# Performance work log

Hardware: AMD Instinct MI355X
Metric: run time of the kernel (lower is better)

The kernel has to match this reference:

```python
import jax, jax.numpy as jnp
import numpy as np

B, T, NM, DM, DI, DS, DR, DC, NC = 8, 512, 128, 512, 1024, 32, 32, 4, 100


def setup_inputs() -> dict:
    ks = jax.random.split(jax.random.key(0), 10)
    r = lambda i, shape, s: (jax.random.normal(ks[i], shape) * s).astype(jnp.float32)
    return {
        "x": jax.random.normal(ks[0], (B, T, NM), dtype=jnp.float32),
        "w_proj": r(1, (NM, DM), 0.05),
        "b_proj": jnp.zeros((DM,), jnp.float32),
        "rms_w": jnp.ones((DM,), jnp.float32),
        "w_in": r(2, (DM, 2 * DI), 0.02),
        "conv_w": r(3, (DI, 1, DC), 0.2),
        "conv_b": jnp.zeros((DI,), jnp.float32),
        "w_xproj": r(4, (DI, DR + 2 * DS), 0.02),
        "w_dt": r(5, (DR, DI), 0.1),
        "b_dt": jnp.full((DI,), -4.6, jnp.float32),  # softplus -> ~0.01 init dt
        "A_log": jnp.log(jnp.broadcast_to(jnp.arange(1, DS + 1, dtype=jnp.float32), (DI, DS))),
        "D": jnp.ones((DI,), jnp.float32),
        "w_out": r(6, (DI, DM), 0.02),
        "w_cls": r(7, (DM, NC), 0.05),
        "b_cls": jnp.zeros((NC,), jnp.float32),
    }


def _forward(x, w_proj, b_proj, rms_w, w_in, conv_w, conv_b, w_xproj, w_dt, b_dt,
             A_log, D, w_out, w_cls, b_cls):
    # LinearNorm input projection: (B,T,NM) -> (B,T,DM)
    h0 = x @ w_proj + b_proj
    # RMSNorm (pre-norm of the ResidualBlock)
    xn = h0 * jax.lax.rsqrt(jnp.mean(h0 * h0, axis=-1, keepdims=True) + 1e-5) * rms_w
    # MambaBlock: in_proj (no bias) -> split into ssm path and gate residual
    xr = xn @ w_in                       # (B,T,2*DI)
    xp, res = jnp.split(xr, 2, axis=-1)  # each (B,T,DI)
    # causal depthwise conv1d (torch pads d_conv-1 both sides then slices [:T])
    xc = jnp.transpose(xp, (0, 2, 1))    # (B,DI,T)
    xc = jax.lax.conv_general_dilated(
        xc, conv_w, window_strides=(1,), padding=((DC - 1, 0),),
        dimension_numbers=("NCH", "OIH", "NCH"), feature_group_count=DI)
    xc = xc + conv_b[None, :, None]
    xp = jax.nn.silu(jnp.transpose(xc, (0, 2, 1)))  # (B,T,DI)
    # input-dependent SSM parameters
    xdbl = xp @ w_xproj                              # (B,T,DR+2*DS)
    dt, Bm, Cm = jnp.split(xdbl, [DR, DR + DS], axis=-1)
    delta = jax.nn.softplus(dt @ w_dt + b_dt)        # (B,T,DI)
    A = -jnp.exp(A_log)                              # (DI,DS)

    # selective scan: h_t = exp(delta_t*A) h_{t-1} + (delta_t*u_t) B_t ; y_t = <h_t, C_t>
    def step(hprev, inp):
        d_t, B_t, C_t, u_t = inp                     # (B,DI),(B,DS),(B,DS),(B,DI)
        dA = jnp.exp(d_t[..., None] * A)             # (B,DI,DS)
        h = dA * hprev + (d_t * u_t)[..., None] * B_t[:, None, :]
        y = jnp.einsum("bds,bs->bd", h, C_t)
        return h, y

    xs = (jnp.swapaxes(delta, 0, 1), jnp.swapaxes(Bm, 0, 1),
          jnp.swapaxes(Cm, 0, 1), jnp.swapaxes(xp, 0, 1))
    h_init = jnp.zeros((B, DI, DS), dtype=x.dtype)
    _, ys = jax.lax.scan(step, h_init, xs)           # ys: (T,B,DI)
    y = jnp.swapaxes(ys, 0, 1) + xp * D              # skip term D*u
    y = y * jax.nn.silu(res)                         # gate
    enc = h0 + y @ w_out                             # residual add
    # NB: faithful to source: mean over dim=2 (feature dim) -> (B,T), T==DM
    pooled = jnp.mean(enc, axis=2)
    return pooled @ w_cls + b_cls                    # (B,NC)


def reference(x, w_proj, b_proj, rms_w, w_in, conv_w, conv_b, w_xproj, w_dt, b_dt,
              A_log, D, w_out, w_cls, b_cls):
    return _forward(x, w_proj, b_proj, rms_w, w_in, conv_w, conv_b, w_xproj,
                    w_dt, b_dt, A_log, D, w_out, w_cls, b_cls)
```

## Files before the change

kernel.cpp:

```cpp
#include <hip/hip_runtime.h>
#include <hip/hip_bf16.h>
#include <cstddef>

#define Bb 8
#define Tt 512
#define NM 128
#define DM 512
#define DI 1024
#define DS 32
#define DR 32
#define DC 4
#define NC 100
#define BT (Bb*Tt)
#define NCH 8
#define CL  64

typedef unsigned short ushort_t;
typedef unsigned int uint_t;
typedef __attribute__((ext_vector_type(8))) short bf8;
typedef __attribute__((ext_vector_type(4))) float f4;

__device__ __forceinline__ float softplus_f(float x) {
    return fmaxf(x, 0.f) + log1pf(expf(-fabsf(x)));
}
__device__ __forceinline__ float silu_fast(float x) {
    return __fdividef(x, 1.f + __expf(-x));
}
__device__ __forceinline__ ushort_t bf16_rne(float x) {
    uint_t u = __float_as_uint(x);
    uint_t r = u + 0x7FFFu + ((u >> 16) & 1u);
    return (ushort_t)(r >> 16);
}
__device__ __forceinline__ float bf16_tof(ushort_t h) {
    return __uint_as_float(((uint_t)h) << 16);
}
__device__ __forceinline__ uint_t packf(float v) {
    ushort_t h = bf16_rne(v);
    ushort_t l = bf16_rne(v - bf16_tof(h));
    return ((uint_t)h << 16) | (uint_t)l;
}
template<int CTRL>
__device__ __forceinline__ float qperm(float x) {
    return __int_as_float(__builtin_amdgcn_mov_dpp(__float_as_int(x), CTRL, 0xF, 0xF, true));
}
template<int PAT>
__device__ __forceinline__ float swz(float x) {
    return __int_as_float(__builtin_amdgcn_ds_swizzle(__float_as_int(x), PAT));
}

__global__ __launch_bounds__(256) void prep_kernel(
    const float* __restrict__ x, const float* __restrict__ w_in,
    const float* __restrict__ w_out, const float* __restrict__ w_xp,
    const float* __restrict__ w_pj, const float* __restrict__ w_dt,
    uint_t* __restrict__ x_pk,
    ushort_t* __restrict__ w_in_hi, ushort_t* __restrict__ w_in_lo,
    ushort_t* __restrict__ w_out_hi, ushort_t* __restrict__ w_out_lo,
    ushort_t* __restrict__ w_xp_hi, ushort_t* __restrict__ w_xp_lo,
    ushort_t* __restrict__ w_pj_hi, ushort_t* __restrict__ w_pj_lo,
    ushort_t* __restrict__ w_dt_hi, ushort_t* __restrict__ w_dt_lo,
    float4* __restrict__ zbase, int zcount)
{
    __shared__ ushort_t th[32][34], tl[32][34];
    const int bid = blockIdx.x;
    const float* src;
    ushort_t *hi, *lo;
    int K, N, bx, by;
    if (bid < 1024)      { src = w_in;  hi = w_in_hi;  lo = w_in_lo;  K = DM; N = 2 * DI; bx = bid & 63; by = bid >> 6; }
    else if (bid < 1536) { const int i = bid - 1024; src = w_out; hi = w_out_hi; lo = w_out_lo; K = DI; N = DM; bx = i & 15; by = i >> 4; }
    else if (bid < 1632) { const int i = bid - 1536; src = w_xp;  hi = w_xp_hi;  lo = w_xp_lo;  K = DI; N = 96; bx = i % 3; by = i / 3; }
    else if (bid < 1696) { const int i = bid - 1632; src = w_pj;  hi = w_pj_hi;  lo = w_pj_lo;  K = NM; N = DM; bx = i & 15; by = i >> 4; }
    else if (bid < 1728) { const int i = bid - 1696; src = w_dt;  hi = w_dt_hi;  lo = w_dt_lo;  K = DR; N = DI; bx = i; by = 0; }
    else {
        const int e = (bid - 1728) * 256 + threadIdx.x;
        x_pk[e] = packf(x[e]);
        if (e < zcount) zbase[e] = make_float4(0.f, 0.f, 0.f, 0.f);
        return;
    }
    const int k0 = by * 32, n0 = bx * 32;
    #pragma unroll
    for (int it = 0; it < 4; ++it) {
        const int idx = it * 256 + threadIdx.x;
        const int r = idx >> 5, c = idx & 31;
        const float v = src[(size_t)(k0 + r) * N + n0 + c];
        const ushort_t h = bf16_rne(v);
        th[c][r] = h;
        tl[c][r] = bf16_rne(v - bf16_tof(h));
    }
    __syncthreads();
    #pragma unroll
    for (int it = 0; it < 4; ++it) {
        const int idx = it * 256 + threadIdx.x;
        const int r = idx >> 5, c = idx & 31;
        hi[(size_t)(n0 + r) * K + k0 + c] = th[r][c];
        lo[(size_t)(n0 + r) * K + k0 + c] = tl[r][c];
    }
}

__global__ __launch_bounds__(512) void gemm_mfma_h0(
    const uint_t* __restrict__ Apk,
    const ushort_t* __restrict__ Bhi, const ushort_t* __restrict__ Blo,
    const float* __restrict__ bias, float* __restrict__ C)
{
    constexpr int BM = 128, BN = 128, FM = 2, FN = 4, K = NM, N = DM;
    __shared__ ushort_t sA[2][BM][40];
    __shared__ ushort_t sB[2][BN][40];
    const int tid = threadIdx.x;
    const int wid = tid >> 6, l = tid & 63, l15 = l & 15, g = l >> 4;
    const int wm = (wid >> 1) * 32, wn = (wid & 1) * 64;
    const int bm0 = blockIdx.y * BM, bn0 = blockIdx.x * BN;

    f4 acc[FM][FN] = {};
    uint4 aR[2], bRh, bRl;

    auto loadG = [&](int k0) {
        #pragma unroll
        for (int r = 0; r < 2; ++r) {
            const int idx = r * 2048 + tid * 4;
            const int m = idx >> 5, k = idx & 31;
            aR[r] = *(const uint4*)(Apk + (size_t)(bm0 + m) * K + k0 + k);
        }
        {
            const int idx = tid * 8;
            const int n = idx >> 5, k = idx & 31;
            const size_t o = (size_t)(bn0 + n) * K + k0 + k;
            bRh = *(const uint4*)(Bhi + o);
            bRl = *(const uint4*)(Blo + o);
        }
    };
    auto stoL = [&]() {
        #pragma unroll
        for (int r = 0; r < 2; ++r) {
            const int idx = r * 2048 + tid * 4;
            const int m = idx >> 5, k = idx & 31;
            uint2 hh, ll;
            hh.x = (aR[r].x >> 16) | (aR[r].y & 0xFFFF0000u);
            hh.y = (aR[r].z >> 16) | (aR[r].w & 0xFFFF0000u);
            ll.x = (aR[r].x & 0xFFFFu) | (aR[r].y << 16);
            ll.y = (aR[r].z & 0xFFFFu) | (aR[r].w << 16);
            *(uint2*)&sA[0][m][k] = hh;
            *(uint2*)&sA[1][m][k] = ll;
        }
        {
            const int idx = tid * 8;
            const int n = idx >> 5, k = idx & 31;
            *(uint4*)&sB[0][n][k] = bRh;
            *(uint4*)&sB[1][n][k] = bRl;
        }
    };

    loadG(0);
    for (int k0 = 0; k0 < K; k0 += 32) {
        stoL();
        __syncthreads();
        if (k0 + 32 < K) loadG(k0 + 32);
        bf8 ah[FM], al_[FM], bh[FN], bl_[FN];
        #pragma unroll
        for (int i = 0; i < FM; ++i) {
            ah[i]  = *(bf8*)&sA[0][wm + i * 16 + l15][g * 8];
            al_[i] = *(bf8*)&sA[1][wm + i * 16 + l15][g * 8];
        }
        #pragma unroll
        for (int j = 0; j < FN; ++j) {
            bh[j]  = *(bf8*)&sB[0][wn + j * 16 + l15][g * 8];
            bl_[j] = *(bf8*)&sB[1][wn + j * 16 + l15][g * 8];
        }
        #pragma unroll
        for (int i = 0; i < FM; ++i)
            #pragma unroll
            for (int j = 0; j < FN; ++j)
                acc[i][j] = __builtin_amdgcn_mfma_f32_16x16x32_bf16(ah[i], bh[j], acc[i][j], 0, 0, 0);
        #pragma unroll
        for (int i = 0; i < FM; ++i)
            #pragma unroll
            for (int j = 0; j < FN; ++j)
                acc[i][j] = __builtin_amdgcn_mfma_f32_16x16x32_bf16(al_[i], bh[j], acc[i][j], 0, 0, 0);
        #pragma unroll
        for (int i = 0; i < FM; ++i)
            #pragma unroll
            for (int j = 0; j < FN; ++j)
                acc[i][j] = __builtin_amdgcn_mfma_f32_16x16x32_bf16(ah[i], bl_[j], acc[i][j], 0, 0, 0);
        __syncthreads();
    }
    #pragma unroll
    for (int i = 0; i < FM; ++i)
        #pragma unroll
        for (int j = 0; j < FN; ++j)
            #pragma unroll
            for (int r = 0; r < 4; ++r) {
                const int m = bm0 + wm + i * 16 + g * 4 + r;
                const int n = bn0 + wn + j * 16 + l15;
                C[(size_t)m * N + n] = acc[i][j][r] + bias[n];
            }
}

__global__ __launch_bounds__(256) void gemm_mfma_dt(
    const float* __restrict__ xdbl,
    const ushort_t* __restrict__ Bhi, const ushort_t* __restrict__ Blo,
    const float* __restrict__ bias, float* __restrict__ dT)
{
    constexpr int FM = 2, FN = 2;
    __shared__ ushort_t sA[2][64][40];
    __shared__ ushort_t sB[2][64][40];
    const int tid = threadIdx.x;
    const int wid = tid >> 6, l = tid & 63, l15 = l & 15, g = l >> 4;
    const int wm = (wid >> 1) * 32, wn = (wid & 1) * 32;
    const int bm0 = blockIdx.y * 64, bn0 = blockIdx.x * 64;

    #pragma unroll
    for (int r = 0; r < 2; ++r) {
        const int idx = r * 1024 + tid * 4;
        const int m = idx >> 5, k = idx & 31;
        const float4 v = *(const float4*)(xdbl + (size_t)(bm0 + m) * 96 + k);
        const float vv[4] = {v.x, v.y, v.z, v.w};
        #pragma unroll
        for (int q = 0; q < 4; ++q) {
            const ushort_t h = bf16_rne(vv[q]);
            sA[0][m][k + q] = h;
            sA[1][m][k + q] = bf16_rne(vv[q] - bf16_tof(h));
        }
    }
    {
        const int idx = tid * 8;
        const int n = idx >> 5, k = idx & 31;
        *(uint4*)&sB[0][n][k] = *(const uint4*)(Bhi + (size_t)(bn0 + n) * 32 + k);
        *(uint4*)&sB[1][n][k] = *(const uint4*)(Blo + (size_t)(bn0 + n) * 32 + k);
    }
    __syncthreads();
    f4 acc[FM][FN] = {};
    bf8 ah[FM], al_[FM], bh[FN], bl_[FN];
    #pragma unroll
    for (int i = 0; i < FM; ++i) {
        ah[i]  = *(bf8*)&sA[0][wm + i * 16 + l15][g * 8];
        al_[i] = *(bf8*)&sA[1][wm + i * 16 + l15][g * 8];
    }
    #pragma unroll
    for (int j = 0; j < FN; ++j) {
        bh[j]  = *(bf8*)&sB[0][wn + j * 16 + l15][g * 8];
        bl_[j] = *(bf8*)&sB[1][wn + j * 16 + l15][g * 8];
    }
    #pragma unroll
    for (int i = 0; i < FM; ++i)
        #pragma unroll
        for (int j = 0; j < FN; ++j) {
            acc[i][j] = __builtin_amdgcn_mfma_f32_16x16x32_bf16(ah[i], bh[j], acc[i][j], 0, 0, 0);
            acc[i][j] = __builtin_amdgcn_mfma_f32_16x16x32_bf16(al_[i], bh[j], acc[i][j], 0, 0, 0);
            acc[i][j] = __builtin_amdgcn_mfma_f32_16x16x32_bf16(ah[i], bl_[j], acc[i][j], 0, 0, 0);
        }
    #pragma unroll
    for (int i = 0; i < FM; ++i)
        #pragma unroll
        for (int j = 0; j < FN; ++j) {
            const int n = bn0 + wn + j * 16 + l15;
            const int m0 = bm0 + wm + i * 16 + g * 4;
            const float bn = bias[n];
            float4 o;
            o.x = softplus_f(acc[i][j][0] + bn);
            o.y = softplus_f(acc[i][j][1] + bn);
            o.z = softplus_f(acc[i][j][2] + bn);
            o.w = softplus_f(acc[i][j][3] + bn);
            *(float4*)(dT + ((size_t)(m0 >> 9) * DI + n) * Tt + (m0 & 511)) = o;
        }
}

__global__ __launch_bounds__(512) void gemm_mfma_big(
    const uint_t* __restrict__ Apk, int lda,
    const ushort_t* __restrict__ Bhi,
    ushort_t* __restrict__ C, int N, int K)
{
    constexpr int FM = 2, FN = 4;
    __shared__ ushort_t sA[128][40];
    __shared__ ushort_t sB[128][40];
    const int tid = threadIdx.x;
    const int wid = tid >> 6, l = tid & 63, l15 = l & 15, g = l >> 4;
    const int wm = (wid >> 1) * 32, wn = (wid & 1) * 64;
    const int bm0 = blockIdx.y * 128, bn0 = blockIdx.x * 128;

    f4 acc[FM][FN] = {};
    uint4 aR[2], bRh;

    auto loadG = [&](int k0) {
        #pragma unroll
        for (int r = 0; r < 2; ++r) {
            const int idx = r * 2048 + tid * 4;
            const int m = idx >> 5, k = idx & 31;
            aR[r] = *(const uint4*)(Apk + (size_t)(bm0 + m) * lda + k0 + k);
        }
        {
            const int idx = tid * 8;
            const int n = idx >> 5, k = idx & 31;
            bRh = *(const uint4*)(Bhi + (size_t)(bn0 + n) * K + k0 + k);
        }
    };
    auto stoL = [&]() {
        #pragma unroll
        for (int r = 0; r < 2; ++r) {
            const int idx = r * 2048 + tid * 4;
            const int m = idx >> 5, k = idx & 31;
            uint2 hh;
            hh.x = (aR[r].x >> 16) | (aR[r].y & 0xFFFF0000u);
            hh.y = (aR[r].z >> 16) | (aR[r].w & 0xFFFF0000u);
            *(uint2*)&sA[m][k] = hh;
        }
        {
            const int idx = tid * 8;
            const int n = idx >> 5, k = idx & 31;
            *(uint4*)&sB[n][k] = bRh;
        }
    };

    loadG(0);
    for (int k0 = 0; k0 < K; k0 += 32) {
        stoL();
        __syncthreads();
        if (k0 + 32 < K) loadG(k0 + 32);
        bf8 ah[FM], bh[FN];
        #pragma unroll
        for (int i = 0; i < FM; ++i)
            ah[i] = *(bf8*)&sA[wm + i * 16 + l15][g * 8];
        #pragma unroll
        for (int j = 0; j < FN; ++j)
            bh[j] = *(bf8*)&sB[wn + j * 16 + l15][g * 8];
        #pragma unroll
        for (int i = 0; i < FM; ++i)
            #pragma unroll
            for (int j = 0; j < FN; ++j)
                acc[i][j] = __builtin_amdgcn_mfma_f32_16x16x32_bf16(ah[i], bh[j], acc[i][j], 0, 0, 0);
        __syncthreads();
    }
    #pragma unroll
    for (int i = 0; i < FM; ++i)
        #pragma unroll
        for (int j = 0; j < FN; ++j)
            #pragma unroll
            for (int r = 0; r < 4; ++r) {
                const int m = bm0 + wm + i * 16 + g * 4 + r;
                const int n = bn0 + wn + j * 16 + l15;
                C[(size_t)m * N + n] = bf16_rne(acc[i][j][r]);
            }
}

__global__ __launch_bounds__(256) void gemm_mfma_x(
    const ushort_t* __restrict__ Abf,
    const ushort_t* __restrict__ Bhi,
    float* __restrict__ C, int K, int kseg)
{
    constexpr int FM = 2, FN = 3;
    __shared__ ushort_t sAx[64][40];
    __shared__ ushort_t sBx[96][40];
    const int tid = threadIdx.x;
    const int wid = tid >> 6, l = tid & 63, l15 = l & 15, g = l >> 4;
    const int wm = (wid >> 1) * 32, wn = (wid & 1) * 48;
    const int bm0 = blockIdx.y * 64;
    const int kbeg = blockIdx.z * kseg;

    f4 acc[FM][FN] = {};
    uint4 aR;
    uint2 bRh[3];

    auto loadG = [&](int k0) {
        {
            const int idx = tid * 8;
            const int m = idx >> 5, k = idx & 31;
            aR = *(const uint4*)(Abf + (size_t)(bm0 + m) * K + k0 + k);
        }
        #pragma unroll
        for (int r = 0; r < 3; ++r) {
            const int idx = r * 1024 + tid * 4;
            const int n = idx >> 5, k = idx & 31;
            bRh[r] = *(const uint2*)(Bhi + (size_t)n * K + k0 + k);
        }
    };
    auto stoL = [&]() {
        {
            const int idx = tid * 8;
            const int m = idx >> 5, k = idx & 31;
            *(uint4*)&sAx[m][k] = aR;
        }
        #pragma unroll
        for (int r = 0; r < 3; ++r) {
            const int idx = r * 1024 + tid * 4;
            const int n = idx >> 5, k = idx & 31;
            *(uint2*)&sBx[n][k] = bRh[r];
        }
    };

    loadG(kbeg);
    for (int k0 = kbeg; k0 < kbeg + kseg; k0 += 32) {
        stoL();
        __syncthreads();
        if (k0 + 32 < kbeg + kseg) loadG(k0 + 32);
        bf8 ah[FM], bh[FN];
        #pragma unroll
        for (int i = 0; i < FM; ++i)
            ah[i] = *(bf8*)&sAx[wm + i * 16 + l15][g * 8];
        #pragma unroll
        for (int j = 0; j < FN; ++j)
            bh[j] = *(bf8*)&sBx[wn + j * 16 + l15][g * 8];
        #pragma unroll
        for (int i = 0; i < FM; ++i)
            #pragma unroll
            for (int j = 0; j < FN; ++j)
                acc[i][j] = __builtin_amdgcn_mfma_f32_16x16x32_bf16(ah[i], bh[j], acc[i][j], 0, 0, 0);
        __syncthreads();
    }
    #pragma unroll
    for (int i = 0; i < FM; ++i)
        #pragma unroll
        for (int j = 0; j < FN; ++j)
            #pragma unroll
            for (int r = 0; r < 4; ++r) {
                const int m = bm0 + wm + i * 16 + g * 4 + r;
                const int n = wn + j * 16 + l15;
                unsafeAtomicAdd(&C[(size_t)m * 96 + n], acc[i][j][r]);
            }
}

__global__ __launch_bounds__(256) void gemm_mfma_pool(
    const uint_t* __restrict__ Apk, int lda,
    const ushort_t* __restrict__ Bhi,
    float* __restrict__ pooled, float pscale,
    int N, int K, int kseg)
{
    constexpr int FM = 2, FN = 2;
    __shared__ ushort_t sA[2][64][40];
    __shared__ ushort_t sB[64][40];
    const int tid = threadIdx.x;
    const int wid = tid >> 6, l = tid & 63, l15 = l & 15, g = l >> 4;
    const int wm = (wid >> 1) * 32, wn = (wid & 1) * 32;
    const int bm0 = blockIdx.y * 64, bn0 = blockIdx.x * 64;
    const int kbeg = blockIdx.z * kseg;

    f4 acc[FM][FN] = {};
    uint4 aR[2], bRh;

    auto loadG = [&](int k0) {
        #pragma unroll
        for (int r = 0; r < 2; ++r) {
            const int idx = r * 1024 + tid * 4;
            const int m = idx >> 5, k = idx & 31;
            aR[r] = *(const uint4*)(Apk + (size_t)(bm0 + m) * lda + k0 + k);
        }
        {
            const int idx = tid * 8;
            const int n = idx >> 5, k = idx & 31;
            bRh = *(const uint4*)(Bhi + (size_t)(bn0 + n) * K + k0 + k);
        }
    };
    auto stoL = [&]() {
        #pragma unroll
        for (int r = 0; r < 2; ++r) {
            const int idx = r * 1024 + tid * 4;
            const int m = idx >> 5, k = idx & 31;
            const uint_t u0 = aR[r].x, u1 = aR[r].y, u2 = aR[r].z, u3 = aR[r].w;
            uint2 hh, ll;
            hh.x = (u0 >> 16) | (u1 & 0xFFFF0000u);
            hh.y = (u2 >> 16) | (u3 & 0xFFFF0000u);
            ll.x = (u0 & 0xFFFFu) | (u1 << 16);
            ll.y = (u2 & 0xFFFFu) | (u3 << 16);
            *(uint2*)&sA[0][m][k] = hh;
            *(uint2*)&sA[1][m][k] = ll;
        }
        {
            const int idx = tid * 8;
            const int n = idx >> 5, k = idx & 31;
            *(uint4*)&sB[n][k] = bRh;
        }
    };

    loadG(kbeg);
    for (int k0 = kbeg; k0 < kbeg + kseg; k0 += 32) {
        stoL();
        __syncthreads();
        if (k0 + 32 < kbeg + kseg) loadG(k0 + 32);
        bf8 ah[FM], al_[FM], bh[FN];
        #pragma unroll
        for (int i = 0; i < FM; ++i) {
            ah[i]  = *(bf8*)&sA[0][wm + i * 16 + l15][g * 8];
            al_[i] = *(bf8*)&sA[1][wm + i * 16 + l15][g * 8];
        }
        #pragma unroll
        for (int j = 0; j < FN; ++j)
            bh[j] = *(bf8*)&sB[wn + j * 16 + l15][g * 8];
        #pragma unroll
        for (int i = 0; i < FM; ++i)
            #pragma unroll
            for (int j = 0; j < FN; ++j)
                acc[i][j] = __builtin_amdgcn_mfma_f32_16x16x32_bf16(ah[i], bh[j], acc[i][j], 0, 0, 0);
        #pragma unroll
        for (int i = 0; i < FM; ++i)
            #pragma unroll
            for (int j = 0; j < FN; ++j)
                acc[i][j] = __builtin_amdgcn_mfma_f32_16x16x32_bf16(al_[i], bh[j], acc[i][j], 0, 0, 0);
        __syncthreads();
    }
    #pragma unroll
    for (int i = 0; i < FM; ++i)
        #pragma unroll
        for (int r = 0; r < 4; ++r) {
            float sum = acc[i][0][r];
            #pragma unroll
            for (int j = 1; j < FN; ++j) sum += acc[i][j][r];
            sum += __shfl_xor(sum, 1);
            sum += __shfl_xor(sum, 2);
            sum += __shfl_xor(sum, 4);
            sum += __shfl_xor(sum, 8);
            if (l15 == 0)
                unsafeAtomicAdd(pooled + bm0 + wm + i * 16 + g * 4 + r, sum * pscale);
        }
}

__global__ __launch_bounds__(256) void rms_kernel(
    const float* __restrict__ h0, const float* __restrict__ w,
    uint_t* __restrict__ xn_pk, float* __restrict__ pooled)
{
    const int row = blockIdx.x;
    const float* p = h0 + (size_t)row * DM;
    const int tid = threadIdx.x;
    float v0 = p[tid], v1 = p[tid + 256];
    float ss = v0 * v0 + v1 * v1;
    float sm = v0 + v1;
    #pragma unroll
    for (int m = 32; m; m >>= 1) {
        ss += __shfl_xor(ss, m);
        sm += __shfl_xor(sm, m);
    }
    __shared__ float wss[4], wsm[4];
    if ((tid & 63) == 0) { wss[tid >> 6] = ss; wsm[tid >> 6] = sm; }
    __syncthreads();
    const float tot = wss[0] + wss[1] + wss[2] + wss[3];
    if (tid == 0)
        unsafeAtomicAdd(pooled + row, (wsm[0] + wsm[1] + wsm[2] + wsm[3]) * (1.0f / DM));
    const float scale = rsqrtf(tot * (1.0f / DM) + 1e-5f);
    xn_pk[(size_t)row * DM + tid]       = packf(v0 * scale * w[tid]);
    xn_pk[(size_t)row * DM + tid + 256] = packf(v1 * scale * w[tid + 256]);
}

__global__ __launch_bounds__(256) void conv_tr_kernel(
    const ushort_t* __restrict__ xr, const float* __restrict__ cw,
    const float* __restrict__ cb, ushort_t* __restrict__ xp_bf,
    ushort_t* __restrict__ res_bf)
{
    __shared__ float tp[64][65];
    __shared__ float tr[64][65];
    const int di0 = blockIdx.x * 64;
    const int t0  = blockIdx.y * 64;
    const int b   = blockIdx.z;
    const int c  = threadIdx.x & 63;
    const int r4 = threadIdx.x >> 6;
    const int di = di0 + c;
    const float bias = cb[di];
    float w0 = cw[di * DC + 0], w1 = cw[di * DC + 1],
          w2 = cw[di * DC + 2], w3 = cw[di * DC + 3];
    #pragma unroll
    for (int rr = 0; rr < 64; rr += 4) {
        const int t = t0 + rr + r4;
        const int bt = b * Tt + t;
        float acc = bias;
        if (t >= 3) {
            acc = fmaf(w0, bf16_tof(xr[(size_t)(bt - 3) * (2 * DI) + di]), acc);
            acc = fmaf(w1, bf16_tof(xr[(size_t)(bt - 2) * (2 * DI) + di]), acc);
            acc = fmaf(w2, bf16_tof(xr[(size_t)(bt - 1) * (2 * DI) + di]), acc);
        } else {
            if (t >= 1) acc = fmaf(w2, bf16_tof(xr[(size_t)(bt - 1) * (2 * DI) + di]), acc);
            if (t >= 2) acc = fmaf(w1, bf16_tof(xr[(size_t)(bt - 2) * (2 * DI) + di]), acc);
        }
        acc = fmaf(w3, bf16_tof(xr[(size_t)bt * (2 * DI) + di]), acc);
        tp[rr + r4][c] = silu_fast(acc);
        tr[rr + r4][c] = bf16_tof(xr[(size_t)bt * (2 * DI) + DI + di]);
    }
    __syncthreads();
    #pragma unroll
    for (int dd = 0; dd < 64; dd += 4) {
        const int dw = dd + r4;
        const size_t o = ((size_t)b * DI + di0 + dw) * Tt + t0 + c;
        xp_bf[o]  = bf16_rne(tp[c][dw]);
        res_bf[o] = bf16_rne(tr[c][dw]);
    }
}

__global__ __launch_bounds__(256) void scan_fused(
    const float* __restrict__ deltaT, const float* __restrict__ xdbl,
    const ushort_t* __restrict__ xp_bf, const ushort_t* __restrict__ res_bf,
    const float* __restrict__ A_log, const float* __restrict__ Dvec,
    uint_t* __restrict__ y_pk)
{
    __shared__ uint_t   sBC[2][DS][68];
    __shared__ float    sD [2][8][68];
    __shared__ float    sDU[2][8][68];
    __shared__ ushort_t sU [2][8][68];
    __shared__ ushort_t sR [2][8][68];
    __shared__ float ylds[CL][9];
    const int tid = threadIdx.x;
    const int grp = tid >> 5;
    const int l5 = tid & 31;
    const int s = ((l5 & 1) << 4) | (l5 >> 1);
    const int b = blockIdx.x >> 7;
    const int di0 = (blockIdx.x & 127) << 3;
    const int sd_r = tid >> 5;
    const int sd_t = (tid & 31) << 1;
    const int bc_t = tid >> 2;
    const int bc_s = (tid & 3) << 3;

    float2 rd2;
    uint_t ru, rr_;
    float4 rB[2], rC[2];
    auto stage_regs = [&](int c) {
        const size_t rb = ((size_t)(b * DI + di0 + sd_r)) * Tt + c * CL + sd_t;
        rd2 = *(const float2*)(deltaT + rb);
        ru  = *(const uint_t*)(xp_bf + rb);
        rr_ = *(const uint_t*)(res_bf + rb);
        const float* src = xdbl + ((size_t)b * Tt + c * CL + bc_t) * 96;
        rB[0] = *(const float4*)(src + 32 + bc_s);
        rB[1] = *(const float4*)(src + 32 + bc_s + 4);
        rC[0] = *(const float4*)(src + 64 + bc_s);
        rC[1] = *(const float4*)(src + 64 + bc_s + 4);
    };
    auto write_lds = [&](int bb) {
        *(float2*)&sD[bb][sd_r][sd_t] = rd2;
        const float u0 = bf16_tof((ushort_t)(ru & 0xFFFFu));
        const float u1 = bf16_tof((ushort_t)(ru >> 16));
        float2 du2;
        du2.x = rd2.x * u0;
        du2.y = rd2.y * u1;
        *(float2*)&sDU[bb][sd_r][sd_t] = du2;
        *(uint_t*)&sU[bb][sd_r][sd_t] = ru;
        *(uint_t*)&sR[bb][sd_r][sd_t] = rr_;
        const float bv[8] = {rB[0].x, rB[0].y, rB[0].z, rB[0].w,
                             rB[1].x, rB[1].y, rB[1].z, rB[1].w};
        const float cv[8] = {rC[0].x, rC[0].y, rC[0].z, rC[0].w,
                             rC[1].x, rC[1].y, rC[1].z, rC[1].w};
        #pragma unroll
        for (int j = 0; j < 8; ++j)
            sBC[bb][bc_s + j][bc_t] =
                ((uint_t)bf16_rne(cv[j]) << 16) | (uint_t)bf16_rne(bv[j]);
    };

    const bool s4b = (l5 & 1) != 0;
    const bool s0b = (l5 & 2) != 0;
    const bool s1b = (l5 & 4) != 0;
    const bool s2b = (l5 & 8) != 0;
    const bool s3b = (l5 & 16) != 0;
    const int di = di0 + grp;
    const float Ads2 = -expf(A_log[di * DS + s]) * 1.44269504f;
    const float Dv = Dvec[di];
    float h = 0.f;

    stage_regs(0);
    write_lds(0);
    #pragma unroll 1
    for (int c = 0; c < NCH; ++c) {
        const int bb = c & 1;
        __syncthreads();
        if (c < NCH - 1) stage_regs(c + 1);
        #pragma unroll 1
        for (int t0 = 0; t0 < CL; t0 += 32) {
            float buf[16] = {};
            uint4 bc_c = *(const uint4*)&sBC[bb][s][t0];
            float4 dv_c = *(const float4*)&sD[bb][grp][t0];
            float4 du_c = *(const float4*)&sDU[bb][grp][t0];
            #pragma unroll
            for (int tq = 0; tq < 8; ++tq) {
                uint4 bc_n;
                float4 dv_n, du_n;
                if (tq < 7) {
                    const int tb = t0 + tq * 4 + 4;
                    bc_n = *(const uint4*)&sBC[bb][s][tb];
                    dv_n = *(const float4*)&sD[bb][grp][tb];
                    du_n = *(const float4*)&sDU[bb][grp][tb];
                }
                const uint_t bcv[4] = {bc_c.x, bc_c.y, bc_c.z, bc_c.w};
                const float dv[4] = {dv_c.x, dv_c.y, dv_c.z, dv_c.w};
                const float duv[4] = {du_c.x, du_c.y, du_c.z, du_c.w};
                #pragma unroll
                for (int q = 0; q < 4; ++q) {
                    const int tl = tq * 4 + q;
                    const float Bq = __uint_as_float(bcv[q] << 16);
                    const float Cq = __uint_as_float(bcv[q] & 0xFFFF0000u);
                    h = fmaf(__builtin_amdgcn_exp2f(dv[q] * Ads2), h, duv[q] * Bq);
                    const float ps = h * Cq;
                    const float pr = ps + qperm<0xB1>(ps);
                    const bool keep = ((tl & 16) != 0) == s4b;
                    buf[tl & 15] = keep ? pr : buf[tl & 15];
                }
                if (tq < 7) { bc_c = bc_n; dv_c = dv_n; du_c = du_n; }
            }
            #pragma unroll
            for (int i = 0; i < 16; ++i) buf[i] += qperm<0x4E>(buf[i]);
            float r8[8];
            #pragma unroll
            for (int i = 0; i < 8; ++i) r8[i] = s0b ? buf[2 * i + 1] : buf[2 * i];
            #pragma unroll
            for (int i = 0; i < 8; ++i) r8[i] += swz<0x101F>(r8[i]);
            float w4[4];
            #pragma unroll
            for (int i = 0; i < 4; ++i) w4[i] = s1b ? r8[2 * i + 1] : r8[2 * i];
            #pragma unroll
            for (int i = 0; i < 4; ++i) w4[i] += swz<0x201F>(w4[i]);
            float v2[2];
            v2[0] = s2b ? w4[1] : w4[0];
            v2[1] = s2b ? w4[3] : w4[2];
            v2[0] += swz<0x401F>(v2[0]);
            v2[1] += swz<0x401F>(v2[1]);
            const float yv = s3b ? v2[1] : v2[0];
            const float uself = bf16_tof(sU[bb][grp][t0 + s]);
            const float rself = bf16_tof(sR[bb][grp][t0 + s]);
            ylds[t0 + s][grp] = fmaf(uself, Dv, yv) * silu_fast(rself);
        }
        __syncthreads();
        {
            const int row = tid >> 2;
            const int q2 = (tid & 3) << 1;
            uint2 o;
            o.x = packf(ylds[row][q2 + 0]);
            o.y = packf(ylds[row][q2 + 1]);
            *(uint2*)(y_pk + ((size_t)b * Tt + c * CL + row) * DI + di0 + q2) = o;
        }
        if (c < NCH - 1) write_lds(bb ^ 1);
    }
}

__global__ __launch_bounds__(256) void cls_kernel(
    const float* __restrict__ pooled, const float* __restrict__ w_cls,
    const float* __restrict__ b_cls, float* __restrict__ out)
{
    const int idx = blockIdx.x * 256 + threadIdx.x;
    if (idx >= Bb * NC) return;
    const int b = idx / NC, c = idx % NC;
    float acc = b_cls[c];
    for (int t = 0; t < DM; ++t)
        acc = fmaf(pooled[b * DM + t], w_cls[t * NC + c], acc);
    out[idx] = acc;
}

extern "C" void kernel_launch(void* const* d_in, const int* in_sizes, int n_in,
                              void* d_out, int out_size, void* d_ws, size_t ws_size,
                              hipStream_t stream) {
    const float* x      = (const float*)d_in[0];
    const float* w_proj = (const float*)d_in[1];
    const float* b_proj = (const float*)d_in[2];
    const float* rms_w  = (const float*)d_in[3];
    const float* w_in   = (const float*)d_in[4];
    const float* conv_w = (const float*)d_in[5];
    const float* conv_b = (const float*)d_in[6];
    const float* w_xprj = (const float*)d_in[7];
    const float* w_dt   = (const float*)d_in[8];
    const float* b_dt   = (const float*)d_in[9];
    const float* A_log  = (const float*)d_in[10];
    const float* Dvec   = (const float*)d_in[11];
    const float* w_out  = (const float*)d_in[12];
    const float* w_cls  = (const float*)d_in[13];
    const float* b_cls  = (const float*)d_in[14];
    float* out = (float*)d_out;

    float* ws = (float*)d_ws;
    float* h0     = ws;
    float* xn     = h0 + (size_t)BT * DM;
    float* xr     = xn + (size_t)BT * DM;
    float* xpT    = xr + (size_t)BT * 2 * DI;
    float* resT   = xpT + (size_t)Bb * DI * Tt;
    float* xdbl   = resT + (size_t)Bb * DI * Tt;
    float* pooled = xdbl + (size_t)BT * 96;
    float* wsplit = pooled + 4096;
    float* deltaT = xr;
    uint_t* y_pk  = (uint_t*)(xr + (size_t)Bb * DI * Tt);
    uint_t* xn_pk = (uint_t*)xn;
    ushort_t* xr_bf  = (ushort_t*)xr;
    ushort_t* xp_bf  = (ushort_t*)xpT;
    ushort_t* res_bf = (ushort_t*)resT;

    ushort_t* w_in_hi  = (ushort_t*)wsplit;
    ushort_t* w_in_lo  = w_in_hi + (size_t)(2 * DI) * DM;
    ushort_t* w_out_hi = w_in_lo + (size_t)(2 * DI) * DM;
    ushort_t* w_out_lo = w_out_hi + (size_t)DM * DI;
    ushort_t* w_xp_hi  = w_out_lo + (size_t)DM * DI;
    ushort_t* w_xp_lo  = w_xp_hi + (size_t)96 * DI;
    ushort_t* w_pj_hi  = w_xp_lo + (size_t)96 * DI;
    ushort_t* w_pj_lo  = w_pj_hi + (size_t)DM * NM;
    ushort_t* w_dt_hi  = w_pj_lo + (size_t)DM * NM;
    ushort_t* w_dt_lo  = w_dt_hi + (size_t)DI * DR;
    uint_t*   x_pk     = (uint_t*)(w_dt_lo + (size_t)DI * DR);

    prep_kernel<<<3776, 256, 0, stream>>>(
        x, w_in, w_out, w_xprj, w_proj, w_dt, x_pk,
        w_in_hi, w_in_lo, w_out_hi, w_out_lo, w_xp_hi, w_xp_lo,
        w_pj_hi, w_pj_lo, w_dt_hi, w_dt_lo,
        (float4*)xdbl, (BT * 96 + 4096) / 4);
    gemm_mfma_h0<<<dim3(DM / 128, BT / 128), 512, 0, stream>>>(
        x_pk, w_pj_hi, w_pj_lo, b_proj, h0);
    rms_kernel<<<BT, 256, 0, stream>>>(h0, rms_w, xn_pk, pooled);
    gemm_mfma_big<<<dim3(2 * DI / 128, BT / 128), 512, 0, stream>>>(
        xn_pk, DM, w_in_hi, xr_bf, 2 * DI, DM);
    conv_tr_kernel<<<dim3(DI / 64, Tt / 64, Bb), 256, 0, stream>>>(
        xr_bf, conv_w, conv_b, xp_bf, res_bf);
    gemm_mfma_x<<<dim3(1, BT / 64, 8), 256, 0, stream>>>(
        xp_bf, w_xp_hi, xdbl, DI, DI / 8);
    gemm_mfma_dt<<<dim3(DI / 64, BT / 64), 256, 0, stream>>>(
        xdbl, w_dt_hi, w_dt_lo, b_dt, deltaT);
    scan_fused<<<Bb * (DI / 8), 256, 0, stream>>>(
        deltaT, xdbl, xp_bf, res_bf, A_log, Dvec, y_pk);
    gemm_mfma_pool<<<dim3(DM / 64, BT / 64, 4), 256, 0, stream>>>(
        y_pk, DI, w_out_hi, pooled, 1.0f / DM, DM, DI, DI / 4);
    cls_kernel<<<(Bb * NC + 255) / 256, 256, 0, stream>>>(pooled, w_cls, b_cls, out);
}
```

Before: 231.3 us.

## Store scan output as plain bf16, drop lo-split MFMA pass, vectorize conv transpose

The scan now writes y as single bf16 values instead of packed hi/lo pairs, so the out-projection/pool GEMM loads half the A data and runs one MFMA pass instead of two. The conv/transpose kernel handles two channels per thread with 32-bit loads and stores, packs bf16 in shared memory, and launches half as many blocks. The h0 GEMM edit only renames constants. Accuracy drops because the lo residual of y is discarded.

```diff
diff --git a/kernel.cpp b/kernel.cpp
--- a/kernel.cpp
+++ b/kernel.cpp
@@ -101,13 +101,14 @@
     const ushort_t* __restrict__ Bhi, const ushort_t* __restrict__ Blo,
     const float* __restrict__ bias, float* __restrict__ C)
 {
-    constexpr int BM = 128, BN = 128, FM = 2, FN = 4, K = NM, N = DM;
-    __shared__ ushort_t sA[2][BM][40];
-    __shared__ ushort_t sB[2][BN][40];
+    constexpr int FM = 2, FN = 4;
+    constexpr int K = NM, N = DM;
+    __shared__ ushort_t sA[2][128][40];
+    __shared__ ushort_t sB[2][128][40];
     const int tid = threadIdx.x;
     const int wid = tid >> 6, l = tid & 63, l15 = l & 15, g = l >> 4;
     const int wm = (wid >> 1) * 32, wn = (wid & 1) * 64;
-    const int bm0 = blockIdx.y * BM, bn0 = blockIdx.x * BN;
+    const int bm0 = blockIdx.y * 128, bn0 = blockIdx.x * 128;
 
     f4 acc[FM][FN] = {};
     uint4 aR[2], bRh, bRl;
@@ -416,13 +417,13 @@
 }
 
 __global__ __launch_bounds__(256) void gemm_mfma_pool(
-    const uint_t* __restrict__ Apk, int lda,
+    const ushort_t* __restrict__ Abf, int lda,
     const ushort_t* __restrict__ Bhi,
     float* __restrict__ pooled, float pscale,
     int N, int K, int kseg)
 {
     constexpr int FM = 2, FN = 2;
-    __shared__ ushort_t sA[2][64][40];
+    __shared__ ushort_t sA[64][40];
     __shared__ ushort_t sB[64][40];
     const int tid = threadIdx.x;
     const int wid = tid >> 6, l = tid & 63, l15 = l & 15, g = l >> 4;
@@ -431,14 +432,13 @@
     const int kbeg = blockIdx.z * kseg;
 
     f4 acc[FM][FN] = {};
-    uint4 aR[2], bRh;
+    uint4 aR, bRh;
 
     auto loadG = [&](int k0) {
-        #pragma unroll
-        for (int r = 0; r < 2; ++r) {
-            const int idx = r * 1024 + tid * 4;
+        {
+            const int idx = tid * 8;
             const int m = idx >> 5, k = idx & 31;
-            aR[r] = *(const uint4*)(Apk + (size_t)(bm0 + m) * lda + k0 + k);
+            aR = *(const uint4*)(Abf + (size_t)(bm0 + m) * lda + k0 + k);
         }
         {
             const int idx = tid * 8;
@@ -447,18 +447,10 @@
         }
     };
     auto stoL = [&]() {
-        #pragma unroll
-        for (int r = 0; r < 2; ++r) {
-            const int idx = r * 1024 + tid * 4;
+        {
+            const int idx = tid * 8;
             const int m = idx >> 5, k = idx & 31;
-            const uint_t u0 = aR[r].x, u1 = aR[r].y, u2 = aR[r].z, u3 = aR[r].w;
-            uint2 hh, ll;
-            hh.x = (u0 >> 16) | (u1 & 0xFFFF0000u);
-            hh.y = (u2 >> 16) | (u3 & 0xFFFF0000u);
-            ll.x = (u0 & 0xFFFFu) | (u1 << 16);
-            ll.y = (u2 & 0xFFFFu) | (u3 << 16);
-            *(uint2*)&sA[0][m][k] = hh;
-            *(uint2*)&sA[1][m][k] = ll;
+            *(uint4*)&sA[m][k] = aR;
         }
         {
             const int idx = tid * 8;
@@ -472,12 +464,10 @@
         stoL();
         __syncthreads();
         if (k0 + 32 < kbeg + kseg) loadG(k0 + 32);
-        bf8 ah[FM], al_[FM], bh[FN];
-        #pragma unroll
-        for (int i = 0; i < FM; ++i) {
-            ah[i]  = *(bf8*)&sA[0][wm + i * 16 + l15][g * 8];
-            al_[i] = *(bf8*)&sA[1][wm + i * 16 + l15][g * 8];
-        }
+        bf8 ah[FM], bh[FN];
+        #pragma unroll
+        for (int i = 0; i < FM; ++i)
+            ah[i] = *(bf8*)&sA[wm + i * 16 + l15][g * 8];
         #pragma unroll
         for (int j = 0; j < FN; ++j)
             bh[j] = *(bf8*)&sB[wn + j * 16 + l15][g * 8];
@@ -486,11 +476,6 @@
             #pragma unroll
             for (int j = 0; j < FN; ++j)
                 acc[i][j] = __builtin_amdgcn_mfma_f32_16x16x32_bf16(ah[i], bh[j], acc[i][j], 0, 0, 0);
-        #pragma unroll
-        for (int i = 0; i < FM; ++i)
-            #pragma unroll
-            for (int j = 0; j < FN; ++j)
-                acc[i][j] = __builtin_amdgcn_mfma_f32_16x16x32_bf16(al_[i], bh[j], acc[i][j], 0, 0, 0);
         __syncthreads();
     }
     #pragma unroll
@@ -540,41 +525,59 @@
     const float* __restrict__ cb, ushort_t* __restrict__ xp_bf,
     ushort_t* __restrict__ res_bf)
 {
-    __shared__ float tp[64][65];
-    __shared__ float tr[64][65];
-    const int di0 = blockIdx.x * 64;
+    __shared__ uint_t sp[64][65];
+    __shared__ uint_t sg[64][65];
+    const int di0 = blockIdx.x * 128;
     const int t0  = blockIdx.y * 64;
     const int b   = blockIdx.z;
-    const int c  = threadIdx.x & 63;
+    const int dp = threadIdx.x & 63;
     const int r4 = threadIdx.x >> 6;
-    const int di = di0 + c;
-    const float bias = cb[di];
-    float w0 = cw[di * DC + 0], w1 = cw[di * DC + 1],
-          w2 = cw[di * DC + 2], w3 = cw[di * DC + 3];
+    const int di = di0 + 2 * dp;
+    const float b0 = cb[di], b1 = cb[di + 1];
+    const float w00 = cw[di * 4 + 0], w01 = cw[di * 4 + 1],
+                w02 = cw[di * 4 + 2], w03 = cw[di * 4 + 3];
+    const float w10 = cw[(di + 1) * 4 + 0], w11 = cw[(di + 1) * 4 + 1],
+                w12 = cw[(di + 1) * 4 + 2], w13 = cw[(di + 1) * 4 + 3];
+    const uint_t* xru = (const uint_t*)xr;
     #pragma unroll
     for (int rr = 0; rr < 64; rr += 4) {
         const int t = t0 + rr + r4;
         const int bt = b * Tt + t;
-        float acc = bias;
-        if (t >= 3) {
-            acc = fmaf(w0, bf16_tof(xr[(size_t)(bt - 3) * (2 * DI) + di]), acc);
-            acc = fmaf(w1, bf16_tof(xr[(size_t)(bt - 2) * (2 * DI) + di]), acc);
-            acc = fmaf(w2, bf16_tof(xr[(size_t)(bt - 1) * (2 * DI) + di]), acc);
-        } else {
-            if (t >= 1) acc = fmaf(w2, bf16_tof(xr[(size_t)(bt - 1) * (2 * DI) + di]), acc);
-            if (t >= 2) acc = fmaf(w1, bf16_tof(xr[(size_t)(bt - 2) * (2 * DI) + di]), acc);
-        }
-        acc = fmaf(w3, bf16_tof(xr[(size_t)bt * (2 * DI) + di]), acc);
-        tp[rr + r4][c] = silu_fast(acc);
-        tr[rr + r4][c] = bf16_tof(xr[(size_t)bt * (2 * DI) + DI + di]);
+        const size_t u3 = (size_t)bt * DI + (di0 >> 1) + dp;
+        const uint_t v3 = xru[u3];
+        const uint_t v2 = (t >= 1) ? xru[u3 - DI] : 0u;
+        const uint_t v1 = (t >= 2) ? xru[u3 - 2 * DI] : 0u;
+        const uint_t v0 = (t >= 3) ? xru[u3 - 3 * DI] : 0u;
+        const uint_t gg = xru[u3 + (DI >> 1)];
+        float a0 = b0, a1 = b1;
+        a0 = fmaf(w00, bf16_tof((ushort_t)v0), a0);
+        a1 = fmaf(w10, bf16_tof((ushort_t)(v0 >> 16)), a1);
+        a0 = fmaf(w01, bf16_tof((ushort_t)v1), a0);
+        a1 = fmaf(w11, bf16_tof((ushort_t)(v1 >> 16)), a1);
+        a0 = fmaf(w02, bf16_tof((ushort_t)v2), a0);
+        a1 = fmaf(w12, bf16_tof((ushort_t)(v2 >> 16)), a1);
+        a0 = fmaf(w03, bf16_tof((ushort_t)v3), a0);
+        a1 = fmaf(w13, bf16_tof((ushort_t)(v3 >> 16)), a1);
+        sp[rr + r4][dp] = (uint_t)bf16_rne(silu_fast(a0)) |
+                          ((uint_t)bf16_rne(silu_fast(a1)) << 16);
+        sg[rr + r4][dp] = gg;
     }
     __syncthreads();
-    #pragma unroll
-    for (int dd = 0; dd < 64; dd += 4) {
-        const int dw = dd + r4;
-        const size_t o = ((size_t)b * DI + di0 + dw) * Tt + t0 + c;
-        xp_bf[o]  = bf16_rne(tp[c][dw]);
-        res_bf[o] = bf16_rne(tr[c][dw]);
+    uint_t* xpo = (uint_t*)xp_bf;
+    uint_t* rso = (uint_t*)res_bf;
+    #pragma unroll
+    for (int it = 0; it < 16; ++it) {
+        const int idx = it * 256 + threadIdx.x;
+        const int dl = idx >> 5;
+        const int tp_ = idx & 31;
+        const int sh = (dl & 1) << 4;
+        const uint_t p0 = (sp[2 * tp_][dl >> 1] >> sh) & 0xFFFFu;
+        const uint_t p1 = (sp[2 * tp_ + 1][dl >> 1] >> sh) & 0xFFFFu;
+        const uint_t g0 = (sg[2 * tp_][dl >> 1] >> sh) & 0xFFFFu;
+        const uint_t g1 = (sg[2 * tp_ + 1][dl >> 1] >> sh) & 0xFFFFu;
+        const size_t o = (((size_t)b * DI + di0 + dl) * Tt + t0 + 2 * tp_) >> 1;
+        xpo[o] = p0 | (p1 << 16);
+        rso[o] = g0 | (g1 << 16);
     }
 }
 
@@ -582,7 +585,7 @@
     const float* __restrict__ deltaT, const float* __restrict__ xdbl,
     const ushort_t* __restrict__ xp_bf, const ushort_t* __restrict__ res_bf,
     const float* __restrict__ A_log, const float* __restrict__ Dvec,
-    uint_t* __restrict__ y_pk)
+    ushort_t* __restrict__ y_bf)
 {
     __shared__ uint_t   sBC[2][DS][68];
     __shared__ float    sD [2][8][68];
@@ -710,10 +713,9 @@
         {
             const int row = tid >> 2;
             const int q2 = (tid & 3) << 1;
-            uint2 o;
-            o.x = packf(ylds[row][q2 + 0]);
-            o.y = packf(ylds[row][q2 + 1]);
-            *(uint2*)(y_pk + ((size_t)b * Tt + c * CL + row) * DI + di0 + q2) = o;
+            const uint_t o = (uint_t)bf16_rne(ylds[row][q2]) |
+                             ((uint_t)bf16_rne(ylds[row][q2 + 1]) << 16);
+            *(uint_t*)(y_bf + ((size_t)b * Tt + c * CL + row) * DI + di0 + q2) = o;
         }
         if (c < NCH - 1) write_lds(bb ^ 1);
     }
@@ -762,7 +764,7 @@
     float* pooled = xdbl + (size_t)BT * 96;
     float* wsplit = pooled + 4096;
     float* deltaT = xr;
-    uint_t* y_pk  = (uint_t*)(xr + (size_t)Bb * DI * Tt);
+    ushort_t* y_bf = (ushort_t*)(xr + (size_t)Bb * DI * Tt);
     uint_t* xn_pk = (uint_t*)xn;
     ushort_t* xr_bf  = (ushort_t*)xr;
     ushort_t* xp_bf  = (ushort_t*)xpT;
@@ -790,15 +792,15 @@
     rms_kernel<<<BT, 256, 0, stream>>>(h0, rms_w, xn_pk, pooled);
     gemm_mfma_big<<<dim3(2 * DI / 128, BT / 128), 512, 0, stream>>>(
         xn_pk, DM, w_in_hi, xr_bf, 2 * DI, DM);
-    conv_tr_kernel<<<dim3(DI / 64, Tt / 64, Bb), 256, 0, stream>>>(
+    conv_tr_kernel<<<dim3(DI / 128, Tt / 64, Bb), 256, 0, stream>>>(
         xr_bf, conv_w, conv_b, xp_bf, res_bf);
     gemm_mfma_x<<<dim3(1, BT / 64, 8), 256, 0, stream>>>(
         xp_bf, w_xp_hi, xdbl, DI, DI / 8);
     gemm_mfma_dt<<<dim3(DI / 64, BT / 64), 256, 0, stream>>>(
         xdbl, w_dt_hi, w_dt_lo, b_dt, deltaT);
     scan_fused<<<Bb * (DI / 8), 256, 0, stream>>>(
-        deltaT, xdbl, xp_bf, res_bf, A_log, Dvec, y_pk);
+        deltaT, xdbl, xp_bf, res_bf, A_log, Dvec, y_bf);
     gemm_mfma_pool<<<dim3(DM / 64, BT / 64, 4), 256, 0, stream>>>(
-        y_pk, DI, w_out_hi, pooled, 1.0f / DM, DM, DI, DI / 4);
+        y_bf, DI, w_out_hi, pooled, 1.0f / DM, DM, DI, DI / 4);
     cls_kernel<<<(Bb * NC + 255) / 256, 256, 0, stream>>>(pooled, w_cls, b_cls, out);
 }
```

Result: faster. 222.6 us (-3.8%).
